# Kernel optimization log

Measured on AMD Instinct MI355X. Metric: run time of the kernel, lower is better.

The kernel has to match this reference:

```python
import jax, jax.numpy as jnp
import numpy as np

N_IN, N_OUT, N_HID, N_RES = 16, 2, 256, 256
B, L = 64, 2048
ALPHA_FAST, ALPHA_SLOW, SIGMA_NEU = 1.0, 0.1, 0.05


def _linear_params(k, n_out, n_in):
    # mimics torch nn.Linear default init: U(-1/sqrt(fan_in), 1/sqrt(fan_in))
    bound = 1.0 / np.sqrt(n_in)
    kw, kb = jax.random.split(k)
    W = jax.random.uniform(kw, (n_out, n_in), minval=-bound, maxval=bound, dtype=jnp.float32)
    b = jax.random.uniform(kb, (n_out,), minval=-bound, maxval=bound, dtype=jnp.float32)
    return W, b


def setup_inputs() -> dict:
    key = jax.random.key(0)
    ks = jax.random.split(key, 11)
    W_in, b_in = _linear_params(ks[0], N_HID, N_IN)
    W_hh, b_hh = _linear_params(ks[1], N_HID, N_HID)
    W_sf, b_sf = _linear_params(ks[2], N_HID, N_RES)
    W_fs, b_fs = _linear_params(ks[3], N_RES, N_HID)
    W_res, b_res = _linear_params(ks[4], N_RES, N_RES)
    W_out, b_out = _linear_params(ks[5], N_OUT, N_HID)
    W_pr, b_pr = _linear_params(ks[6], N_IN, N_RES)
    input_signal = jax.random.normal(ks[7], (B, L, N_IN), dtype=jnp.float32)
    hidden = jax.random.normal(ks[8], (B, N_HID), dtype=jnp.float32)
    reservoir = jax.random.normal(ks[9], (B, N_RES), dtype=jnp.float32)
    # neural noise: randn * sigma_neu * sqrt(alpha_fast), precomputed time-major [L,B,H]
    noise = jax.random.normal(ks[10], (L, B, N_HID), dtype=jnp.float32) * (SIGMA_NEU * np.sqrt(ALPHA_FAST))
    return dict(input_signal=input_signal, hidden=hidden, reservoir=reservoir, noise=noise,
                W_in=W_in, b_in=b_in, W_hh=W_hh, b_hh=b_hh, W_sf=W_sf, b_sf=b_sf,
                W_fs=W_fs, b_fs=b_fs, W_res=W_res, b_res=b_res,
                W_out=W_out, b_out=b_out, W_pr=W_pr, b_pr=b_pr, length=L)


def reference(input_signal, hidden, reservoir, noise,
              W_in, b_in, W_hh, b_hh, W_sf, b_sf, W_fs, b_fs,
              W_res, b_res, W_out, b_out, W_pr, b_pr, length):
    xs = jnp.transpose(input_signal, (1, 0, 2))  # [L, B, n_in], time-major like torch permute
    af = jnp.float32(ALPHA_FAST)
    asl = jnp.float32(ALPHA_SLOW)

    def step(carry, inp):
        h, r = carry
        x_t, nz = inp
        tmp_h = jax.nn.relu(x_t @ W_in.T + b_in + h @ W_hh.T + b_hh + r @ W_sf.T + b_sf)
        tmp_r = jax.nn.relu(h @ W_fs.T + b_fs + r @ W_res.T + b_res)
        h = (1.0 - af) * h + af * tmp_h + nz
        r = (1.0 - asl) * r + asl * tmp_r
        out = jnp.clip(h @ W_out.T + b_out, -2.0, 2.0)
        prior = jax.nn.sigmoid(r @ W_pr.T + b_pr)
        return (h, r), (h, out, prior)

    _, (hs, outs, priors) = jax.lax.scan(step, (hidden, reservoir), (xs, noise))
    # back to batch-major [B, L, .]
    return (jnp.transpose(hs, (1, 0, 2)),
            jnp.transpose(outs, (1, 0, 2)),
            jnp.transpose(priors, (1, 0, 2)))
```

## Files before the change

### kernel.cpp

```cpp
#include <hip/hip_runtime.h>
#include <stdint.h>
#include <stddef.h>

#define LT    2048
#define BATCH 64
#define NH    256
#define HS_ELEMS  (BATCH * LT * NH)
#define OUT_ELEMS (BATCH * LT * 2)

typedef __attribute__((ext_vector_type(8))) __bf16 bf16x8;
typedef __attribute__((ext_vector_type(4))) float  f32x4;
typedef __attribute__((ext_vector_type(2))) unsigned u32x2;

static __device__ __forceinline__ unsigned pk2(float a, float b) {
  unsigned r;
  asm("v_cvt_pk_bf16_f32 %0, %1, %2" : "=v"(r) : "v"(a), "v"(b));
  return r;
}
static __device__ __forceinline__ bf16x8 pack8v(f32x4 a, f32x4 b) {
  union { unsigned u[4]; bf16x8 v; } r;
  r.u[0] = pk2(a[0], a[1]); r.u[1] = pk2(a[2], a[3]);
  r.u[2] = pk2(b[0], b[1]); r.u[3] = pk2(b[2], b[3]);
  return r.v;
}
static __device__ __forceinline__ bf16x8 pack8(const float* p) {
  return pack8v(*(const f32x4*)p, *(const f32x4*)(p + 4));
}

#define BARRIER() do {                                           \
    asm volatile("s_waitcnt lgkmcnt(0)" ::: "memory");           \
    __builtin_amdgcn_s_barrier();                                \
    asm volatile("" ::: "memory");                               \
  } while (0)

#define W_RES_OFF 0
#define A_S_OFF   131072
#define W_PR_OFF  147456
#define BIASR_OFF 155648
#define BP_OFF    156672
#define LDS_BYTES 156736

__global__ __launch_bounds__(256) void u_precompute_kernel(
    const float* __restrict__ x,
    const float* __restrict__ W_in,
    const float* __restrict__ b_in,
    const float* __restrict__ b_hh,
    const float* __restrict__ b_sf,
    float* __restrict__ u)
{
  __shared__ float xs[64][16];
  const int tid = threadIdx.x;
  const int b  = blockIdx.x >> 5;
  const int tc = (blockIdx.x & 31) << 6;
  float w[16];
#pragma unroll
  for (int i = 0; i < 16; ++i) w[i] = W_in[tid * 16 + i];
  const float bias = b_in[tid] + b_hh[tid] + b_sf[tid];
  for (int r = tid; r < 64 * 16; r += 256)
    xs[r >> 4][r & 15] = x[((size_t)b * LT + tc + (r >> 4)) * 16 + (r & 15)];
  __syncthreads();
  for (int tt = 0; tt < 64; ++tt) {
    float s = bias;
#pragma unroll
    for (int i = 0; i < 16; ++i) s += xs[tt][i] * w[i];
    u[((size_t)b * LT + tc + tt) * NH + tid] = s;
  }
}

__global__ __launch_bounds__(512, 1) void rnn_seq_kernel(
    const float* __restrict__ hidden,
    const float* __restrict__ reservoir,
    const float* __restrict__ noise,
    const float* __restrict__ W_hh, const float* __restrict__ W_sf,
    const float* __restrict__ W_fs, const float* __restrict__ W_res,
    const float* __restrict__ b_fs, const float* __restrict__ b_res,
    const float* __restrict__ W_pr, const float* __restrict__ b_pr,
    float* __restrict__ hs,
    float* __restrict__ priors)
{
  extern __shared__ char lds[];
  const int tid  = threadIdx.x;
  const int lane = tid & 63;
  const int wv   = tid >> 6;
  const int col  = lane & 15;
  const int kg   = lane >> 4;
  const int b0   = blockIdx.x * 16;

#pragma unroll 4
  for (int j = 0; j < 16; ++j) {
    const int c   = j * 512 + tid;
    const int kk8 = c >> 10, n = (c >> 2) & 255, kgs = c & 3;
    *(bf16x8*)(lds + W_RES_OFF + c * 16) =
        pack8(W_res + (size_t)n * NH + kk8 * 32 + kgs * 8);
  }
  {
    const int kk8 = tid >> 6, l16 = tid & 63;
    const int kgs = l16 >> 4, n = l16 & 15;
    *(bf16x8*)(lds + W_PR_OFF + tid * 16) =
        pack8(W_pr + (size_t)n * NH + kk8 * 32 + kgs * 8);
  }
  {
    const int kk = tid >> 6, l16 = tid & 63;
    const int kgs = l16 >> 4, m = l16 & 15;
    *(bf16x8*)(lds + A_S_OFF + tid * 16) =
        pack8(hidden + (size_t)(b0 + m) * NH + kk * 32 + kgs * 8);
    *(bf16x8*)(lds + A_S_OFF + (tid + 512) * 16) =
        pack8(reservoir + (size_t)(b0 + m) * NH + kk * 32 + kgs * 8);
  }
  if (tid < 64) {
    f32x4 v = *(const f32x4*)(b_fs + tid * 4);
    f32x4 w = *(const f32x4*)(b_res + tid * 4);
    *(f32x4*)(lds + BIASR_OFF + tid * 16) = v + w;
  }
  if (tid < 4)
    *(f32x4*)(lds + BP_OFF + tid * 16) = *(const f32x4*)(b_pr + tid * 4);

  bf16x8 wHH[2][8], wSF[2][8], wFS[2][8];
#pragma unroll
  for (int tile = 0; tile < 2; ++tile) {
    const int n = wv * 32 + tile * 16 + col;
#pragma unroll
    for (int kk = 0; kk < 8; ++kk) {
      wHH[tile][kk] = pack8(W_hh + (size_t)n * NH + kk * 32 + kg * 8);
      wSF[tile][kk] = pack8(W_sf + (size_t)n * NH + kk * 32 + kg * 8);
      wFS[tile][kk] = pack8(W_fs + (size_t)n * NH + kk * 32 + kg * 8);
    }
  }

  const size_t hsRow = (size_t)(b0 + col) * (LT * NH);
  const size_t nzRow = (size_t)(b0 + col) * NH;
  f32x4 r_old[2], accH[2], accR[2], accP;
#pragma unroll
  for (int tile = 0; tile < 2; ++tile) {
    const int nb = wv * 32 + tile * 16 + kg * 4;
    r_old[tile] = *(const f32x4*)(reservoir + nzRow + nb);
    accH[tile]  = *(const f32x4*)(hs + hsRow + nb);
    accR[tile]  = *(const f32x4*)(lds + BIASR_OFF + nb * 4);
  }
  accP = *(const f32x4*)(lds + BP_OFF + kg * 16);

  BARRIER();

#pragma unroll 1
  for (int t = 0; t < LT; ++t) {
    const size_t tp1 = (t + 1 < LT) ? (size_t)(t + 1) : (size_t)(LT - 1);
    f32x4 pfU[2], nzc[2];
#pragma unroll
    for (int tile = 0; tile < 2; ++tile) {
      const int nb = wv * 32 + tile * 16 + kg * 4;
      pfU[tile] = *(const f32x4*)(hs + hsRow + tp1 * NH + nb);
      nzc[tile] = *(const f32x4*)(noise + (size_t)t * (BATCH * NH) + nzRow + nb);
    }

    const char* afp = lds + A_S_OFF + lane * 16;
    const char* bwp = lds + W_RES_OFF + (wv * 32) * 64 + col * 64 + kg * 16;
    const char* bpp = lds + W_PR_OFF + lane * 16;
#pragma unroll
    for (int kk = 0; kk < 16; ++kk) {
      const bf16x8 af = *(const bf16x8*)(afp + kk * 1024);
      if (kk < 8) {
#pragma unroll
        for (int tile = 0; tile < 2; ++tile)
          accH[tile] = __builtin_amdgcn_mfma_f32_16x16x32_bf16(wHH[tile][kk], af, accH[tile], 0, 0, 0);
#pragma unroll
        for (int tile = 0; tile < 2; ++tile)
          accR[tile] = __builtin_amdgcn_mfma_f32_16x16x32_bf16(wFS[tile][kk], af, accR[tile], 0, 0, 0);
      } else {
#pragma unroll
        for (int tile = 0; tile < 2; ++tile)
          accH[tile] = __builtin_amdgcn_mfma_f32_16x16x32_bf16(wSF[tile][kk - 8], af, accH[tile], 0, 0, 0);
#pragma unroll
        for (int tile = 0; tile < 2; ++tile) {
          const bf16x8 bw = *(const bf16x8*)(bwp + (kk - 8) * 16384 + tile * 1024);
          accR[tile] = __builtin_amdgcn_mfma_f32_16x16x32_bf16(bw, af, accR[tile], 0, 0, 0);
        }
        if (wv == 1) {
          const bf16x8 bp = *(const bf16x8*)(bpp + (kk - 8) * 1024);
          accP = __builtin_amdgcn_mfma_f32_16x16x32_bf16(bp, af, accP, 0, 0, 0);
        }
      }
    }
    BARRIER();

    float* hsT = hs + hsRow + (size_t)t * NH;
    char* abase = lds + A_S_OFF + wv * 1024 + col * 16 + (kg & 1) * 8;
#pragma unroll
    for (int tile = 0; tile < 2; ++tile) {
      const int nb = wv * 32 + tile * 16 + kg * 4;
      f32x4 hv, rv;
#pragma unroll
      for (int j = 0; j < 4; ++j) {
        hv[j] = fmaxf(accH[tile][j], 0.f) + nzc[tile][j];
        rv[j] = 0.9f * r_old[tile][j] + 0.1f * fmaxf(accR[tile][j], 0.f);
      }
      r_old[tile] = rv;
      *(f32x4*)(hsT + nb) = hv;
      u32x2 hp, rp;
      hp[0] = pk2(hv[0], hv[1]); hp[1] = pk2(hv[2], hv[3]);
      rp[0] = pk2(rv[0], rv[1]); rp[1] = pk2(rv[2], rv[3]);
      char* dst = abase + (2 * tile + (kg >> 1)) * 256;
      *(u32x2*)dst          = hp;
      *(u32x2*)(dst + 8192) = rp;
    }
    if (wv == 1 && t > 0) {
      f32x4 pv;
#pragma unroll
      for (int j = 0; j < 4; ++j) pv[j] = 1.f / (1.f + __expf(-accP[j]));
      *(f32x4*)(priors + (size_t)(b0 + col) * (LT * 16) + (size_t)(t - 1) * 16 + kg * 4) = pv;
    }

#pragma unroll
    for (int tile = 0; tile < 2; ++tile) {
      const int nb = wv * 32 + tile * 16 + kg * 4;
      accH[tile] = pfU[tile];
      accR[tile] = *(const f32x4*)(lds + BIASR_OFF + nb * 4);
    }
    accP = *(const f32x4*)(lds + BP_OFF + kg * 16);
    BARRIER();
  }

  if (wv == 1) {
    f32x4 aP = *(const f32x4*)(lds + BP_OFF + kg * 16);
    const char* afp = lds + A_S_OFF + 8192 + lane * 16;
    const char* bpp = lds + W_PR_OFF + lane * 16;
#pragma unroll
    for (int kk8 = 0; kk8 < 8; ++kk8) {
      const bf16x8 af = *(const bf16x8*)(afp + kk8 * 1024);
      const bf16x8 bp = *(const bf16x8*)(bpp + kk8 * 1024);
      aP = __builtin_amdgcn_mfma_f32_16x16x32_bf16(bp, af, aP, 0, 0, 0);
    }
    f32x4 pv;
#pragma unroll
    for (int j = 0; j < 4; ++j) pv[j] = 1.f / (1.f + __expf(-aP[j]));
    *(f32x4*)(priors + (size_t)(b0 + col) * (LT * 16) + (size_t)(LT - 1) * 16 + kg * 4) = pv;
  }
}

__global__ __launch_bounds__(256) void out_project_kernel(
    const float* __restrict__ hs,
    const float* __restrict__ W_out,
    const float* __restrict__ b_out,
    float* __restrict__ outs)
{
  const int tid = threadIdx.x;
  const int lane = tid & 63;
  const int wv = tid >> 6;
  const int row0 = blockIdx.x * 64 + wv * 16;
  f32x4 w0 = *(const f32x4*)(W_out + lane * 4);
  f32x4 w1 = *(const f32x4*)(W_out + 256 + lane * 4);
  const float bo0 = b_out[0], bo1 = b_out[1];
  for (int i = 0; i < 16; ++i) {
    const f32x4 h = *(const f32x4*)(hs + (size_t)(row0 + i) * NH + lane * 4);
    float p0 = h[0]*w0[0] + h[1]*w0[1] + h[2]*w0[2] + h[3]*w0[3];
    float p1 = h[0]*w1[0] + h[1]*w1[1] + h[2]*w1[2] + h[3]*w1[3];
#pragma unroll
    for (int off = 32; off; off >>= 1) {
      p0 += __shfl_down(p0, off, 64);
      p1 += __shfl_down(p1, off, 64);
    }
    if (lane == 0) {
      const size_t o = (size_t)(row0 + i) * 2;
      outs[o]     = fminf(fmaxf(p0 + bo0, -2.f), 2.f);
      outs[o + 1] = fminf(fmaxf(p1 + bo1, -2.f), 2.f);
    }
  }
}

extern "C" void kernel_launch(void* const* d_in, const int* in_sizes, int n_in,
                              void* d_out, int out_size, void* d_ws, size_t ws_size,
                              hipStream_t stream) {
  const float* x         = (const float*)d_in[0];
  const float* hidden    = (const float*)d_in[1];
  const float* reservoir = (const float*)d_in[2];
  const float* noise     = (const float*)d_in[3];
  const float* W_in      = (const float*)d_in[4];
  const float* b_in      = (const float*)d_in[5];
  const float* W_hh      = (const float*)d_in[6];
  const float* b_hh      = (const float*)d_in[7];
  const float* W_sf      = (const float*)d_in[8];
  const float* b_sf      = (const float*)d_in[9];
  const float* W_fs      = (const float*)d_in[10];
  const float* b_fs      = (const float*)d_in[11];
  const float* W_res     = (const float*)d_in[12];
  const float* b_res     = (const float*)d_in[13];
  const float* W_out     = (const float*)d_in[14];
  const float* b_out     = (const float*)d_in[15];
  const float* W_pr      = (const float*)d_in[16];
  const float* b_pr      = (const float*)d_in[17];

  float* hs     = (float*)d_out;
  float* outs   = hs + HS_ELEMS;
  float* priors = outs + OUT_ELEMS;

  u_precompute_kernel<<<2048, 256, 0, stream>>>(x, W_in, b_in, b_hh, b_sf, hs);

  hipFuncSetAttribute((const void*)rnn_seq_kernel,
                      hipFuncAttributeMaxDynamicSharedMemorySize, LDS_BYTES);
  rnn_seq_kernel<<<4, 512, LDS_BYTES, stream>>>(
      hidden, reservoir, noise, W_hh, W_sf, W_fs, W_res,
      b_fs, b_res, W_pr, b_pr, hs, priors);

  out_project_kernel<<<2048, 256, 0, stream>>>(hs, W_out, b_out, outs);
}
```

Baseline: 6.000 ms.

## Double-buffer recurrent state in LDS to drop one barrier per timestep

Splits the bf16 h/r activation buffer in LDS into two ping-pong halves indexed by timestep parity. Each step reads one half and writes the other, so the barrier between the MFMA reads and the state writes can go, leaving a single barrier per step. W_pr and the combined biases also move from LDS into registers, and launch bounds change to (512,2). The costs are more register pressure, which the new launch bound may make worse and lead to spills, and a final-step prior read that must pick the correct buffer half.

```diff
diff --git a/kernel.cpp b/kernel.cpp
--- a/kernel.cpp
+++ b/kernel.cpp
@@ -34,11 +34,9 @@
   } while (0)
 
 #define W_RES_OFF 0
-#define A_S_OFF   131072
-#define W_PR_OFF  147456
-#define BIASR_OFF 155648
-#define BP_OFF    156672
-#define LDS_BYTES 156736
+#define A_S0_OFF  131072
+#define A_S1_OFF  147456
+#define LDS_BYTES 163840
 
 __global__ __launch_bounds__(256) void u_precompute_kernel(
     const float* __restrict__ x,
@@ -67,7 +65,7 @@
   }
 }
 
-__global__ __launch_bounds__(512, 1) void rnn_seq_kernel(
+__global__ __launch_bounds__(512, 2) void rnn_seq_kernel(
     const float* __restrict__ hidden,
     const float* __restrict__ reservoir,
     const float* __restrict__ noise,
@@ -94,28 +92,16 @@
         pack8(W_res + (size_t)n * NH + kk8 * 32 + kgs * 8);
   }
   {
-    const int kk8 = tid >> 6, l16 = tid & 63;
-    const int kgs = l16 >> 4, n = l16 & 15;
-    *(bf16x8*)(lds + W_PR_OFF + tid * 16) =
-        pack8(W_pr + (size_t)n * NH + kk8 * 32 + kgs * 8);
-  }
-  {
     const int kk = tid >> 6, l16 = tid & 63;
     const int kgs = l16 >> 4, m = l16 & 15;
-    *(bf16x8*)(lds + A_S_OFF + tid * 16) =
+    *(bf16x8*)(lds + A_S0_OFF + tid * 16) =
         pack8(hidden + (size_t)(b0 + m) * NH + kk * 32 + kgs * 8);
-    *(bf16x8*)(lds + A_S_OFF + (tid + 512) * 16) =
+    *(bf16x8*)(lds + A_S0_OFF + (tid + 512) * 16) =
         pack8(reservoir + (size_t)(b0 + m) * NH + kk * 32 + kgs * 8);
   }
-  if (tid < 64) {
-    f32x4 v = *(const f32x4*)(b_fs + tid * 4);
-    f32x4 w = *(const f32x4*)(b_res + tid * 4);
-    *(f32x4*)(lds + BIASR_OFF + tid * 16) = v + w;
-  }
-  if (tid < 4)
-    *(f32x4*)(lds + BP_OFF + tid * 16) = *(const f32x4*)(b_pr + tid * 4);
-
-  bf16x8 wHH[2][8], wSF[2][8], wFS[2][8];
+
+  bf16x8 wHH[2][8], wSF[2][8], wFS[2][8], wPR[8];
+  f32x4 biasrR[2];
 #pragma unroll
   for (int tile = 0; tile < 2; ++tile) {
     const int n = wv * 32 + tile * 16 + col;
@@ -125,7 +111,15 @@
       wSF[tile][kk] = pack8(W_sf + (size_t)n * NH + kk * 32 + kg * 8);
       wFS[tile][kk] = pack8(W_fs + (size_t)n * NH + kk * 32 + kg * 8);
     }
-  }
+    const int nb = wv * 32 + tile * 16 + kg * 4;
+    f32x4 bf = *(const f32x4*)(b_fs + nb);
+    f32x4 br = *(const f32x4*)(b_res + nb);
+    biasrR[tile] = bf + br;
+  }
+#pragma unroll
+  for (int kk8 = 0; kk8 < 8; ++kk8)
+    wPR[kk8] = pack8(W_pr + (size_t)col * NH + kk8 * 32 + kg * 8);
+  const f32x4 bp4 = *(const f32x4*)(b_pr + kg * 4);
 
   const size_t hsRow = (size_t)(b0 + col) * (LT * NH);
   const size_t nzRow = (size_t)(b0 + col) * NH;
@@ -135,9 +129,9 @@
     const int nb = wv * 32 + tile * 16 + kg * 4;
     r_old[tile] = *(const f32x4*)(reservoir + nzRow + nb);
     accH[tile]  = *(const f32x4*)(hs + hsRow + nb);
-    accR[tile]  = *(const f32x4*)(lds + BIASR_OFF + nb * 4);
-  }
-  accP = *(const f32x4*)(lds + BP_OFF + kg * 16);
+    accR[tile]  = biasrR[tile];
+  }
+  accP = bp4;
 
   BARRIER();
 
@@ -152,9 +146,9 @@
       nzc[tile] = *(const f32x4*)(noise + (size_t)t * (BATCH * NH) + nzRow + nb);
     }
 
-    const char* afp = lds + A_S_OFF + lane * 16;
+    const char* aRd = lds + A_S0_OFF + (t & 1) * 16384;
+    const char* afp = aRd + lane * 16;
     const char* bwp = lds + W_RES_OFF + (wv * 32) * 64 + col * 64 + kg * 16;
-    const char* bpp = lds + W_PR_OFF + lane * 16;
 #pragma unroll
     for (int kk = 0; kk < 16; ++kk) {
       const bf16x8 af = *(const bf16x8*)(afp + kk * 1024);
@@ -175,15 +169,14 @@
           accR[tile] = __builtin_amdgcn_mfma_f32_16x16x32_bf16(bw, af, accR[tile], 0, 0, 0);
         }
         if (wv == 1) {
-          const bf16x8 bp = *(const bf16x8*)(bpp + (kk - 8) * 1024);
-          accP = __builtin_amdgcn_mfma_f32_16x16x32_bf16(bp, af, accP, 0, 0, 0);
+          accP = __builtin_amdgcn_mfma_f32_16x16x32_bf16(wPR[kk - 8], af, accP, 0, 0, 0);
         }
       }
     }
-    BARRIER();
 
     float* hsT = hs + hsRow + (size_t)t * NH;
-    char* abase = lds + A_S_OFF + wv * 1024 + col * 16 + (kg & 1) * 8;
+    char* abase = lds + A_S0_OFF + ((t + 1) & 1) * 16384 +
+                  wv * 1024 + col * 16 + (kg & 1) * 8;
 #pragma unroll
     for (int tile = 0; tile < 2; ++tile) {
       const int nb = wv * 32 + tile * 16 + kg * 4;
@@ -211,23 +204,20 @@
 
 #pragma unroll
     for (int tile = 0; tile < 2; ++tile) {
-      const int nb = wv * 32 + tile * 16 + kg * 4;
       accH[tile] = pfU[tile];
-      accR[tile] = *(const f32x4*)(lds + BIASR_OFF + nb * 4);
-    }
-    accP = *(const f32x4*)(lds + BP_OFF + kg * 16);
+      accR[tile] = biasrR[tile];
+    }
+    accP = bp4;
     BARRIER();
   }
 
   if (wv == 1) {
-    f32x4 aP = *(const f32x4*)(lds + BP_OFF + kg * 16);
-    const char* afp = lds + A_S_OFF + 8192 + lane * 16;
-    const char* bpp = lds + W_PR_OFF + lane * 16;
+    f32x4 aP = bp4;
+    const char* afp = lds + A_S0_OFF + 8192 + lane * 16;
 #pragma unroll
     for (int kk8 = 0; kk8 < 8; ++kk8) {
       const bf16x8 af = *(const bf16x8*)(afp + kk8 * 1024);
-      const bf16x8 bp = *(const bf16x8*)(bpp + kk8 * 1024);
-      aP = __builtin_amdgcn_mfma_f32_16x16x32_bf16(bp, af, aP, 0, 0, 0);
+      aP = __builtin_amdgcn_mfma_f32_16x16x32_bf16(wPR[kk8], af, aP, 0, 0, 0);
     }
     f32x4 pv;
 #pragma unroll
```

Measured after the change: 9.983 ms. 66.4% more time.
